# Optimization experiments

Hardware: AMD Instinct MI355X
Metric: run time of the kernel (lower is better)

## Reference

```python
import jax, jax.numpy as jnp
import numpy as np

TOPK = 0.1   # effective steady-state topk (target_topk)
TAU = 0.0    # topk_tau default: pure sparse output


def setup_inputs() -> dict:
    key = jax.random.key(0)
    x = jax.random.normal(key, (64, 256, 64, 64), dtype=jnp.float32)
    return {"x": x}


def reference(x):
    # sparse_hw: keep top-k |value| positions over the H*W axis per (n, c) row.
    n, c, h, w = x.shape
    hw = h * w
    k = int(max(1, TOPK * hw))  # 409 for 64x64 at topk=0.1
    xr = x.reshape(n, c, hw)
    # torch.topk(x_reshape.abs(), k, dim=2) -> indices of k largest magnitudes
    _, idx = jax.lax.top_k(jnp.abs(xr), k)  # idx: [n, c, k]
    # mask = zeros.scatter_(2, idx, 1)
    mask = jnp.zeros_like(xr).at[
        jnp.arange(n)[:, None, None],
        jnp.arange(c)[None, :, None],
        idx,
    ].set(1.0)
    sparse_x = (mask * xr).reshape(n, c, h, w)
    if TAU == 0.0:
        return sparse_x
    # tau blend: tau * x + (1 - tau) * sparse_x
    return TAU * x + (1.0 - TAU) * sparse_x
```

## Files before the change

### kernel.cpp

```cpp
#include <hip/hip_runtime.h>

#define HW_ 4096
#define KSEL 409
#define LDSW 4128

template<int NBINS, int NCOPIES, int STRIDE>
__device__ __forceinline__ void radix_scan(const unsigned* lds, volatile unsigned* sb,
                                           unsigned kneed, int t) {
  constexpr int C = NBINS / 256;
  unsigned hsum[C];
  #pragma unroll
  for (int j = 0; j < C; ++j) hsum[j] = 0;
  #pragma unroll
  for (int c = 0; c < NCOPIES; ++c) {
    #pragma unroll
    for (int q = 0; q < C / 4; ++q) {
      uint4 u = *(const uint4*)&lds[c * STRIDE + C * t + 4 * q];
      hsum[4*q+0] += u.x; hsum[4*q+1] += u.y; hsum[4*q+2] += u.z; hsum[4*q+3] += u.w;
    }
  }
  unsigned val = 0;
  #pragma unroll
  for (int j = 0; j < C; ++j) val += hsum[j];
  const int lane = t & 63, w = t >> 6;
  unsigned inc = val;
  #pragma unroll
  for (int off = 1; off < 64; off <<= 1) {
    unsigned u = __shfl_down(inc, off);
    if (lane + off < 64) inc += u;
  }
  if (lane == 0) sb[4 + w] = inc;
  __syncthreads();
  unsigned above_waves = 0;
  #pragma unroll
  for (int w2 = 0; w2 < 4; ++w2) if (w2 > w) above_waves += sb[4 + w2];
  const unsigned P = inc + above_waves;
  unsigned cum = P - val;
  if (cum < kneed && kneed <= P) {
    #pragma unroll
    for (int j = C - 1; j >= 0; --j) {
      unsigned h = hsum[j];
      if (cum + h >= kneed) { sb[0] = C * t + j; sb[1] = kneed - cum; sb[2] = h; break; }
      cum += h;
    }
  }
  __syncthreads();
}

extern "C" __global__ void __launch_bounds__(256, 6)
topk_kern(const float* __restrict__ x, float* __restrict__ out) {
  __shared__ unsigned lds[LDSW];
  __shared__ unsigned sb[8];
  const int t = threadIdx.x;
  const int w = t >> 6;
  const size_t rowoff = (size_t)blockIdx.x * HW_;
  const float4* xr = (const float4*)(x + rowoff);
  float4* orow = (float4*)(out + rowoff);

  float4 v[4];
  #pragma unroll
  for (int j = 0; j < 4; ++j) v[j] = xr[t + j * 256];
  const float* pv = (const float*)v;

  #pragma unroll
  for (int c = 0; c < 4; ++c)
    #pragma unroll
    for (int j = 0; j < 4; ++j) lds[c * 1032 + t + j * 256] = 0;
  __syncthreads();
  {
    unsigned* myh = &lds[w * 1032];
    #pragma unroll
    for (int i = 0; i < 16; ++i) {
      unsigned ab = __float_as_uint(pv[i]) & 0x7FFFFFFFu;
      atomicAdd(&myh[ab >> 21], 1u);
    }
  }
  __syncthreads();
  radix_scan<1024, 4, 1032>(lds, sb, KSEL, t);
  const unsigned b1 = sb[0];
  const unsigned k2 = sb[1];

  #pragma unroll
  for (int c = 0; c < 2; ++c)
    #pragma unroll
    for (int j = 0; j < 8; ++j) lds[c * 2056 + t + j * 256] = 0;
  __syncthreads();
  {
    unsigned* myh = &lds[(w >> 1) * 2056];
    #pragma unroll
    for (int i = 0; i < 16; ++i) {
      unsigned ab = __float_as_uint(pv[i]) & 0x7FFFFFFFu;
      if ((ab >> 21) == b1) atomicAdd(&myh[(ab >> 10) & 0x7FFu], 1u);
    }
  }
  __syncthreads();
  radix_scan<2048, 2, 2056>(lds, sb, k2, t);
  const unsigned b2 = sb[0];
  const unsigned k3 = sb[1];
  const unsigned P21 = (b1 << 11) | b2;

  #pragma unroll
  for (int c = 0; c < 4; ++c)
    #pragma unroll
    for (int j = 0; j < 4; ++j) lds[c * 1032 + t + j * 256] = 0;
  __syncthreads();
  {
    unsigned* myh = &lds[w * 1032];
    #pragma unroll
    for (int i = 0; i < 16; ++i) {
      unsigned ab = __float_as_uint(pv[i]) & 0x7FFFFFFFu;
      if ((ab >> 10) == P21) atomicAdd(&myh[ab & 0x3FFu], 1u);
    }
  }
  __syncthreads();
  radix_scan<1024, 4, 1032>(lds, sb, k3, t);
  const unsigned b3 = sb[0];
  const unsigned rem = sb[1];
  const unsigned ceq = sb[2];
  const unsigned T = (P21 << 10) | b3;

  unsigned keep = 0;
  #pragma unroll
  for (int i = 0; i < 16; ++i) {
    unsigned ab = __float_as_uint(pv[i]) & 0x7FFFFFFFu;
    if (ab > T) keep |= (1u << i);
  }

  if (rem == ceq) {
    #pragma unroll
    for (int i = 0; i < 16; ++i) {
      unsigned ab = __float_as_uint(pv[i]) & 0x7FFFFFFFu;
      if (ab == T) keep |= (1u << i);
    }
  } else {
    __syncthreads();
    unsigned* eqh = (unsigned*)lds;
    #pragma unroll
    for (int j = 0; j < 4; ++j) {
      unsigned c = 0;
      #pragma unroll
      for (int e = 0; e < 4; ++e)
        if ((__float_as_uint(pv[4*j+e]) & 0x7FFFFFFFu) == T) ++c;
      eqh[j * 256 + t] = c;
    }
    __syncthreads();
    if (t == 0) {
      unsigned run = 0;
      for (int i = 0; i < 1024; ++i) { unsigned h = eqh[i]; eqh[i] = run; run += h; }
    }
    __syncthreads();
    #pragma unroll
    for (int j = 0; j < 4; ++j) {
      unsigned r = eqh[j * 256 + t];
      #pragma unroll
      for (int e = 0; e < 4; ++e) {
        if ((__float_as_uint(pv[4*j+e]) & 0x7FFFFFFFu) == T) {
          if (r < rem) keep |= (1u << (4*j + e));
          ++r;
        }
      }
    }
  }

  #pragma unroll
  for (int j = 0; j < 4; ++j) {
    float4 o;
    o.x = ((keep >> (4*j+0)) & 1u) ? v[j].x : 0.0f;
    o.y = ((keep >> (4*j+1)) & 1u) ? v[j].y : 0.0f;
    o.z = ((keep >> (4*j+2)) & 1u) ? v[j].z : 0.0f;
    o.w = ((keep >> (4*j+3)) & 1u) ? v[j].w : 0.0f;
    orow[t + j * 256] = o;
  }
}

extern "C" void kernel_launch(void* const* d_in, const int* in_sizes, int n_in,
                              void* d_out, int out_size, void* d_ws, size_t ws_size,
                              hipStream_t stream) {
  const float* x = (const float*)d_in[0];
  float* out = (float*)d_out;
  const int rows = in_sizes[0] / HW_;
  topk_kern<<<dim3(rows), dim3(256), 0, stream>>>(x, out);
}
```

Measured before the change: 432.4 us.

## Prefilter values above fixed threshold and restructure radix passes with single histograms

```diff
diff --git a/kernel.cpp b/kernel.cpp
--- a/kernel.cpp
+++ b/kernel.cpp
@@ -2,22 +2,17 @@
 
 #define HW_ 4096
 #define KSEL 409
-#define LDSW 4128
+#define T0BITS 0x3FC00000u
 
-template<int NBINS, int NCOPIES, int STRIDE>
-__device__ __forceinline__ void radix_scan(const unsigned* lds, volatile unsigned* sb,
+template<int NBINS>
+__device__ __forceinline__ void radix_scan(const unsigned* hist, volatile unsigned* sb,
                                            unsigned kneed, int t) {
   constexpr int C = NBINS / 256;
   unsigned hsum[C];
   #pragma unroll
-  for (int j = 0; j < C; ++j) hsum[j] = 0;
-  #pragma unroll
-  for (int c = 0; c < NCOPIES; ++c) {
-    #pragma unroll
-    for (int q = 0; q < C / 4; ++q) {
-      uint4 u = *(const uint4*)&lds[c * STRIDE + C * t + 4 * q];
-      hsum[4*q+0] += u.x; hsum[4*q+1] += u.y; hsum[4*q+2] += u.z; hsum[4*q+3] += u.w;
-    }
+  for (int q = 0; q < C / 4; ++q) {
+    uint4 u = *(const uint4*)&hist[C * t + 4 * q];
+    hsum[4*q+0] = u.x; hsum[4*q+1] = u.y; hsum[4*q+2] = u.z; hsum[4*q+3] = u.w;
   }
   unsigned val = 0;
   #pragma unroll
@@ -47,73 +42,65 @@
   __syncthreads();
 }
 
-extern "C" __global__ void __launch_bounds__(256, 6)
+extern "C" __global__ void __launch_bounds__(256, 5)
 topk_kern(const float* __restrict__ x, float* __restrict__ out) {
-  __shared__ unsigned lds[LDSW];
+  __shared__ unsigned h1[2048];
+  __shared__ unsigned h2[1024];
+  __shared__ unsigned h3[1024];
   __shared__ unsigned sb[8];
   const int t = threadIdx.x;
-  const int w = t >> 6;
+  const int lane = t & 63, w = t >> 6;
   const size_t rowoff = (size_t)blockIdx.x * HW_;
   const float4* xr = (const float4*)(x + rowoff);
   float4* orow = (float4*)(out + rowoff);
 
   float4 v[4];
+  unsigned ab[16];
   #pragma unroll
-  for (int j = 0; j < 4; ++j) v[j] = xr[t + j * 256];
-  const float* pv = (const float*)v;
+  for (int j = 0; j < 4; ++j) {
+    v[j] = xr[t + j * 256];
+    ab[4*j+0] = __float_as_uint(v[j].x) & 0x7FFFFFFFu;
+    ab[4*j+1] = __float_as_uint(v[j].y) & 0x7FFFFFFFu;
+    ab[4*j+2] = __float_as_uint(v[j].z) & 0x7FFFFFFFu;
+    ab[4*j+3] = __float_as_uint(v[j].w) & 0x7FFFFFFFu;
+  }
+
+  *(uint4*)&h1[4 * t] = make_uint4(0, 0, 0, 0);
+  *(uint4*)&h1[4 * t + 1024] = make_uint4(0, 0, 0, 0);
+  *(uint4*)&h2[4 * t] = make_uint4(0, 0, 0, 0);
+  *(uint4*)&h3[4 * t] = make_uint4(0, 0, 0, 0);
+  unsigned cnt = 0;
+  #pragma unroll
+  for (int i = 0; i < 16; ++i) cnt += (ab[i] > T0BITS) ? 1u : 0u;
+  #pragma unroll
+  for (int off = 1; off < 64; off <<= 1) cnt += __shfl_down(cnt, off);
+  if (lane == 0) sb[4 + w] = cnt;
+  __syncthreads();
+  const unsigned c0 = sb[4] + sb[5] + sb[6] + sb[7];
+  const bool filt = (c0 >= KSEL);
 
   #pragma unroll
-  for (int c = 0; c < 4; ++c)
-    #pragma unroll
-    for (int j = 0; j < 4; ++j) lds[c * 1032 + t + j * 256] = 0;
+  for (int i = 0; i < 16; ++i)
+    if (!filt || ab[i] > T0BITS) atomicAdd(&h1[ab[i] >> 20], 1u);
   __syncthreads();
-  {
-    unsigned* myh = &lds[w * 1032];
-    #pragma unroll
-    for (int i = 0; i < 16; ++i) {
-      unsigned ab = __float_as_uint(pv[i]) & 0x7FFFFFFFu;
-      atomicAdd(&myh[ab >> 21], 1u);
-    }
-  }
-  __syncthreads();
-  radix_scan<1024, 4, 1032>(lds, sb, KSEL, t);
+  radix_scan<2048>(h1, sb, KSEL, t);
   const unsigned b1 = sb[0];
   const unsigned k2 = sb[1];
 
   #pragma unroll
-  for (int c = 0; c < 2; ++c)
-    #pragma unroll
-    for (int j = 0; j < 8; ++j) lds[c * 2056 + t + j * 256] = 0;
+  for (int i = 0; i < 16; ++i)
+    if ((ab[i] >> 20) == b1) atomicAdd(&h2[(ab[i] >> 10) & 0x3FFu], 1u);
   __syncthreads();
-  {
-    unsigned* myh = &lds[(w >> 1) * 2056];
-    #pragma unroll
-    for (int i = 0; i < 16; ++i) {
-      unsigned ab = __float_as_uint(pv[i]) & 0x7FFFFFFFu;
-      if ((ab >> 21) == b1) atomicAdd(&myh[(ab >> 10) & 0x7FFu], 1u);
-    }
-  }
-  __syncthreads();
-  radix_scan<2048, 2, 2056>(lds, sb, k2, t);
+  radix_scan<1024>(h2, sb, k2, t);
   const unsigned b2 = sb[0];
   const unsigned k3 = sb[1];
-  const unsigned P21 = (b1 << 11) | b2;
+  const unsigned P21 = (b1 << 10) | b2;
 
   #pragma unroll
-  for (int c = 0; c < 4; ++c)
-    #pragma unroll
-    for (int j = 0; j < 4; ++j) lds[c * 1032 + t + j * 256] = 0;
+  for (int i = 0; i < 16; ++i)
+    if ((ab[i] >> 10) == P21) atomicAdd(&h3[ab[i] & 0x3FFu], 1u);
   __syncthreads();
-  {
-    unsigned* myh = &lds[w * 1032];
-    #pragma unroll
-    for (int i = 0; i < 16; ++i) {
-      unsigned ab = __float_as_uint(pv[i]) & 0x7FFFFFFFu;
-      if ((ab >> 10) == P21) atomicAdd(&myh[ab & 0x3FFu], 1u);
-    }
-  }
-  __syncthreads();
-  radix_scan<1024, 4, 1032>(lds, sb, k3, t);
+  radix_scan<1024>(h3, sb, k3, t);
   const unsigned b3 = sb[0];
   const unsigned rem = sb[1];
   const unsigned ceq = sb[2];
@@ -121,26 +108,19 @@
 
   unsigned keep = 0;
   #pragma unroll
-  for (int i = 0; i < 16; ++i) {
-    unsigned ab = __float_as_uint(pv[i]) & 0x7FFFFFFFu;
-    if (ab > T) keep |= (1u << i);
-  }
+  for (int i = 0; i < 16; ++i) if (ab[i] > T) keep |= (1u << i);
 
   if (rem == ceq) {
     #pragma unroll
-    for (int i = 0; i < 16; ++i) {
-      unsigned ab = __float_as_uint(pv[i]) & 0x7FFFFFFFu;
-      if (ab == T) keep |= (1u << i);
-    }
+    for (int i = 0; i < 16; ++i) if (ab[i] == T) keep |= (1u << i);
   } else {
     __syncthreads();
-    unsigned* eqh = (unsigned*)lds;
+    unsigned* eqh = h1;
     #pragma unroll
     for (int j = 0; j < 4; ++j) {
       unsigned c = 0;
       #pragma unroll
-      for (int e = 0; e < 4; ++e)
-        if ((__float_as_uint(pv[4*j+e]) & 0x7FFFFFFFu) == T) ++c;
+      for (int e = 0; e < 4; ++e) if (ab[4*j+e] == T) ++c;
       eqh[j * 256 + t] = c;
     }
     __syncthreads();
@@ -154,10 +134,7 @@
       unsigned r = eqh[j * 256 + t];
       #pragma unroll
       for (int e = 0; e < 4; ++e) {
-        if ((__float_as_uint(pv[4*j+e]) & 0x7FFFFFFFu) == T) {
-          if (r < rem) keep |= (1u << (4*j + e));
-          ++r;
-        }
+        if (ab[4*j+e] == T) { if (r < rem) keep |= (1u << (4*j + e)); ++r; }
       }
     }
   }
```

Measured after the change: 428.0 us. Within noise of the previous version (-1.0%).
